# Optimization experiments

Measured on AMD Instinct MI355X. Metric: run time of the kernel, lower is better.

The kernel has to match this reference:

```python
import jax, jax.numpy as jnp
import numpy as np

VOCAB = 100000
EMB = 256
HID = 512
H = HID // 2            # per-direction hidden size
T_LEN = 2048
N_TAGS = 7
START, END = 5, 6
NEG = -10000.0


def setup_inputs() -> dict:
    key = jax.random.key(0)
    ks = jax.random.split(key, 16)
    n = lambda k, sh: jax.random.normal(k, sh, dtype=jnp.float32)
    bound = 1.0 / np.sqrt(H)  # torch LSTM/Linear-style init scale
    u = lambda k, sh: jax.random.uniform(k, sh, dtype=jnp.float32, minval=-bound, maxval=bound)
    transitions = n(ks[12], (N_TAGS, N_TAGS))
    transitions = transitions.at[:, START].set(NEG).at[END, :].set(NEG)
    return {
        "words": jax.random.randint(ks[0], (T_LEN,), 0, VOCAB),
        "embed": n(ks[1], (VOCAB + 1, EMB)),
        "W_ih_f": u(ks[2], (4 * H, EMB)),
        "W_hh_f": u(ks[3], (4 * H, H)),
        "b_ih_f": u(ks[4], (4 * H,)),
        "b_hh_f": u(ks[5], (4 * H,)),
        "W_ih_b": u(ks[6], (4 * H, EMB)),
        "W_hh_b": u(ks[7], (4 * H, H)),
        "b_ih_b": u(ks[8], (4 * H,)),
        "b_hh_b": u(ks[9], (4 * H,)),
        "W_out": u(ks[10], (N_TAGS, HID)),
        "b_out": u(ks[11], (N_TAGS,)),
        "transitions": transitions,
        "h0": n(ks[13], (2, H)),
        "c0": n(ks[14], (2, H)),
    }


def _lstm_dir(xs, h0, c0, Wih, Whh, bih, bhh):
    # xs: [T, EMB]; torch gate order i, f, g, o
    def step(carry, x):
        h, c = carry
        g = x @ Wih.T + bih + h @ Whh.T + bhh  # [4H]
        i, f, gg, o = jnp.split(g, 4)
        i, f, o = jax.nn.sigmoid(i), jax.nn.sigmoid(f), jax.nn.sigmoid(o)
        c = f * c + i * jnp.tanh(gg)
        h = o * jnp.tanh(c)
        return (h, c), h
    _, hs = jax.lax.scan(step, (h0, c0), xs)
    return hs  # [T, H]


def _features(words, embed, W_ih_f, W_hh_f, b_ih_f, b_hh_f,
              W_ih_b, W_hh_b, b_ih_b, b_hh_b, W_out, b_out, h0, c0):
    xs = embed[words]                                   # [T, EMB]
    hs_f = _lstm_dir(xs, h0[0], c0[0], W_ih_f, W_hh_f, b_ih_f, b_hh_f)
    hs_b = _lstm_dir(xs[::-1], h0[1], c0[1], W_ih_b, W_hh_b, b_ih_b, b_hh_b)[::-1]
    lstm_out = jnp.concatenate([hs_f, hs_b], axis=1)    # [T, HID]
    return lstm_out @ W_out.T + b_out                   # [T, N_TAGS]


def _viterbi(feats, transitions):
    init = jnp.full((N_TAGS,), NEG, dtype=feats.dtype).at[START].set(0.0)

    def vit_step(fv, feat):
        # torch code: next_tag_var[j] = forward_var + transitions[j]
        M = fv[None, :] + transitions          # [j, i] = fv[i] + T[j, i]
        bp = jnp.argmax(M, axis=1)             # [N_TAGS] best prev tag
        fv_new = jnp.max(M, axis=1) + feat
        return fv_new, bp

    fv, bptrs = jax.lax.scan(vit_step, init, feats)     # bptrs: [T, N_TAGS]
    terminal = fv + transitions[END]
    final_tag = jnp.argmax(terminal)
    path_score = terminal[final_tag]

    def back_step(tag, bp):
        return bp[tag], tag
    _start, path = jax.lax.scan(back_step, final_tag, bptrs, reverse=True)
    return path_score, path  # path: [T] tag ids (B/I/E/S/N = 0..4)


def reference(words, embed, W_ih_f, W_hh_f, b_ih_f, b_hh_f,
              W_ih_b, W_hh_b, b_ih_b, b_hh_b, W_out, b_out,
              transitions, h0, c0):
    feats = _features(words, embed, W_ih_f, W_hh_f, b_ih_f, b_hh_f,
                      W_ih_b, W_hh_b, b_ih_b, b_hh_b, W_out, b_out, h0, c0)
    return _viterbi(feats, transitions)
```

## Files before the change

kernel.cpp:

```cpp
#include <hip/hip_runtime.h>

typedef unsigned int u32;
typedef int v4i __attribute__((ext_vector_type(4)));

#define T_LEN 2048
#define NEG (-10000.0f)
#define WSCALE 2032.0f
#define HSCALE 127.0f
#define SCALE_INV (1.0f / (2032.0f * 127.0f))

__device__ __forceinline__ u32 rdlane_u32(u32 v, int lane) {
#if __has_builtin(__builtin_amdgcn_readlane)
  return (u32)__builtin_amdgcn_readlane((int)v, lane);
#else
  return (u32)__shfl((int)v, lane);
#endif
}

__device__ __forceinline__ float rdlane_f32(float v, int lane) {
  return __builtin_bit_cast(float, rdlane_u32(__builtin_bit_cast(u32, v), lane));
}

__device__ __forceinline__ void block_sync_lds() {
  asm volatile("s_waitcnt lgkmcnt(0)" ::: "memory");
  __builtin_amdgcn_s_barrier();
}

__device__ __forceinline__ v4i mfma_i8(v4i a, v4i b, v4i c) {
#if __has_builtin(__builtin_amdgcn_mfma_i32_16x16x64_i8)
  return __builtin_amdgcn_mfma_i32_16x16x64_i8(a, b, c, 0, 0, 0);
#else
  v4i d;
  asm("v_mfma_i32_16x16x64_i8 %0, %1, %2, %3"
      : "=&v"(d) : "v"(a), "v"(b), "v"(c));
  return d;
#endif
}

__global__ void pack_whh_i8(const float* __restrict__ Wf,
                            const float* __restrict__ Wb,
                            u32* __restrict__ WP) {
  int idx = blockIdx.x * 256 + threadIdx.x;
  int e  = idx & 3;
  int l  = (idx >> 2) & 63;
  int kt = (idx >> 8) & 3;
  int rt = (idx >> 10) & 63;
  int d  = (idx >> 16) & 1;
  int row = rt * 16 + (l & 15);
  int k0  = kt * 64 + (l >> 4) * 16 + e * 4;
  const float* W = d ? Wb : Wf;
  u32 p = 0;
  #pragma unroll
  for (int b = 0; b < 4; ++b) {
    float x = W[row * 256 + k0 + b];
    int q = (int)rintf(fminf(fmaxf(x * WSCALE, -127.f), 127.f));
    p |= (u32)(q & 255) << (8 * b);
  }
  WP[idx] = p;
}

__global__ void gather_kernel(const int* __restrict__ words,
                              const float* __restrict__ embed,
                              float* __restrict__ xs) {
  int t = blockIdx.x;
  int k = threadIdx.x;
  xs[t * 256 + k] = embed[(size_t)words[t] * 256 + k];
}

__global__ __launch_bounds__(256) void gemm_xw(
    const float* __restrict__ xs,
    const float* __restrict__ Wf, const float* __restrict__ Wb,
    const float* __restrict__ bihf, const float* __restrict__ bhhf,
    const float* __restrict__ bihb, const float* __restrict__ bhhb,
    float* __restrict__ XW) {
  __shared__ float lx[32 * 256];
  __shared__ float lw[32 * 132];
  const int tid = threadIdx.x;
  const int t0 = blockIdx.x * 32;
  const int g0 = blockIdx.y * 128;
  const int d  = blockIdx.z;
  const float* W = d ? Wb : Wf;

  #pragma unroll 4
  for (int r = 0; r < 32; ++r) lx[r * 256 + tid] = xs[(t0 + r) * 256 + tid];

  const int tg = tid & 31, tt = tid >> 5;
  float acc[4][4] = {};

  for (int kc = 0; kc < 8; ++kc) {
    __syncthreads();
    #pragma unroll
    for (int r2 = 0; r2 < 16; ++r2) {
      int gg = r2 * 8 + (tid >> 5);
      int k  = tid & 31;
      lw[k * 132 + gg] = W[(g0 + gg) * 256 + kc * 32 + k];
    }
    __syncthreads();
    #pragma unroll
    for (int k = 0; k < 32; ++k) {
      float4 wv = *(const float4*)&lw[k * 132 + tg * 4];
      #pragma unroll
      for (int a = 0; a < 4; ++a) {
        float xa = lx[(tt * 4 + a) * 256 + kc * 32 + k];
        acc[a][0] = fmaf(xa, wv.x, acc[a][0]);
        acc[a][1] = fmaf(xa, wv.y, acc[a][1]);
        acc[a][2] = fmaf(xa, wv.z, acc[a][2]);
        acc[a][3] = fmaf(xa, wv.w, acc[a][3]);
      }
    }
  }
  const float* bih = d ? bihb : bihf;
  const float* bhh = d ? bhhb : bhhf;
  int gcol = g0 + tg * 4;
  float bb[4];
  #pragma unroll
  for (int j = 0; j < 4; ++j) bb[j] = bih[gcol + j] + bhh[gcol + j];
  #pragma unroll
  for (int a = 0; a < 4; ++a) {
    size_t trow = (size_t)d * T_LEN + t0 + tt * 4 + a;
    #pragma unroll
    for (int j = 0; j < 4; ++j) {
      int g = gcol + j;
      XW[trow * 1024 + (g & 255) * 4 + (g >> 8)] = acc[a][j] + bb[j];
    }
  }
}

__global__ void __launch_bounds__(512)
__attribute__((amdgpu_waves_per_eu(2, 2)))
lstm_seq(
    const float* __restrict__ XW, float* __restrict__ HS,
    const u32* __restrict__ wpack,
    const float* __restrict__ h0, const float* __restrict__ c0) {
  __shared__ u32 smem[1152];
  const int t = threadIdx.x;
  const int d = blockIdx.x;
  const int lane = t & 63;
  const int w = t >> 6;
  const int c = t & 255;

  v4i A[8][4];
  {
    const v4i* AP = (const v4i*)wpack;
    #pragma unroll
    for (int j = 0; j < 8; ++j) {
      #pragma unroll
      for (int kt = 0; kt < 4; ++kt)
        A[j][kt] = AP[((d * 64 + w * 8 + j) * 4 + kt) * 64 + lane];
    }
  }

  unsigned char* H8b = (unsigned char*)smem;
  float cst = 0.f, h = 0.f;
  if (t < 256) {
    cst = c0[d * 256 + c];
    h   = h0[d * 256 + c];
    int hi = (int)rintf(fminf(fmaxf(h, -1.f), 1.f) * HSCALE);
    H8b[c] = (unsigned char)(hi & 255);
  }
  block_sync_lds();

  const char* sb = (const char*)smem;
  const int gq = (lane >> 4) * 16;
  char* gtp = (char*)smem + 512 + w * 512 + gq;

  const int delta = d ? -1024 : 1024;
  const float* xwp = XW + ((size_t)d * T_LEN + (d ? (T_LEN - 1) : 0)) * 1024 + c * 4;
  float4 xc = make_float4(0.f, 0.f, 0.f, 0.f);
  if (t < 256) xc = *(const float4*)xwp;

  for (int s = 0; s < T_LEN; ++s) {
    float4 xn = make_float4(0.f, 0.f, 0.f, 0.f);
    if (t < 256 && s < T_LEN - 1) { xwp += delta; xn = *(const float4*)xwp; }

    const char* hp = sb + (s & 1) * 256 + gq;
    v4i B0 = *(const v4i*)(hp);
    v4i B1 = *(const v4i*)(hp + 64);
    v4i B2 = *(const v4i*)(hp + 128);
    v4i B3 = *(const v4i*)(hp + 192);

    v4i D[8];
    #pragma unroll
    for (int j = 0; j < 8; ++j) {
      v4i acc = {0, 0, 0, 0};
      acc = mfma_i8(A[j][0], B0, acc);
      acc = mfma_i8(A[j][1], B1, acc);
      acc = mfma_i8(A[j][2], B2, acc);
      acc = mfma_i8(A[j][3], B3, acc);
      D[j] = acc;
    }
    if ((lane & 15) == 0) {
      #pragma unroll
      for (int j = 0; j < 8; ++j)
        *(v4i*)(gtp + j * 64) = D[j];
    }
    block_sync_lds();

    if (t < 256) {
      int aI = *(const int*)(sb + 512  + c * 4);
      int aF = *(const int*)(sb + 1536 + c * 4);
      int aG = *(const int*)(sb + 2560 + c * 4);
      int aO = *(const int*)(sb + 3584 + c * 4);
      float gi = fmaf((float)aI, SCALE_INV, xc.x);
      float gf = fmaf((float)aF, SCALE_INV, xc.y);
      float gc = fmaf((float)aG, SCALE_INV, xc.z);
      float go = fmaf((float)aO, SCALE_INV, xc.w);
      gi = 1.f / (1.f + __expf(-gi));
      gf = 1.f / (1.f + __expf(-gf));
      go = 1.f / (1.f + __expf(-go));
      gc = 1.f - 2.f / (__expf(2.f * gc) + 1.f);
      cst = gf * cst + gi * gc;
      float th = 1.f - 2.f / (__expf(2.f * cst) + 1.f);
      h = go * th;
      int hi = (int)rintf(h * HSCALE);
      H8b[((s + 1) & 1) * 256 + c] = (unsigned char)(hi & 255);
      const int tt = d ? (T_LEN - 1 - s) : s;
      HS[((size_t)d * T_LEN + tt) * 256 + c] = h;
    }
    block_sync_lds();
    xc = xn;
  }
}

__global__ void feats_kernel(const float* __restrict__ hs,
                             const float* __restrict__ wout,
                             const float* __restrict__ bout,
                             float* __restrict__ feats) {
  __shared__ float lf[16 * 257];
  __shared__ float lb[16 * 257];
  const int tid = threadIdx.x;
  const int t0 = blockIdx.x * 16;
  for (int i = tid; i < 16 * 256; i += 128) {
    int r = i >> 8, k = i & 255;
    lf[r * 257 + k] = hs[(size_t)(t0 + r) * 256 + k];
    lb[r * 257 + k] = hs[(size_t)T_LEN * 256 + (size_t)(t0 + r) * 256 + k];
  }
  __syncthreads();
  const int tl = tid >> 3, n = tid & 7;
  if (n < 7) {
    float acc = bout[n];
    #pragma unroll 8
    for (int k = 0; k < 256; ++k) acc = fmaf(lf[tl * 257 + k], wout[n * 512 + k], acc);
    #pragma unroll 8
    for (int k = 0; k < 256; ++k) acc = fmaf(lb[tl * 257 + k], wout[n * 512 + 256 + k], acc);
    feats[(t0 + tl) * 7 + n] = acc;
  }
}

__global__ __launch_bounds__(256) void viterbi_kernel(
    const float* __restrict__ feats,
    const float* __restrict__ trans,
    float* __restrict__ out) {
  extern __shared__ char vsm[];
  float*         fe = (float*)vsm;
  unsigned char* bp = (unsigned char*)(vsm + 57344);
  unsigned char* G  = (unsigned char*)(vsm + 73728);
  unsigned char* bt = (unsigned char*)(vsm + 73984);
  const int tid = threadIdx.x;

  for (int i = tid; i < T_LEN * 7; i += 256) fe[i] = feats[i];
  __syncthreads();

  if (tid < 64) {
    const int j  = tid;
    const int jc = (j < 7) ? j : 0;
    float Trow[7];
    #pragma unroll
    for (int i = 0; i < 7; ++i) Trow[i] = trans[jc * 7 + i];
    float fv = (j == 5) ? 0.0f : NEG;
    for (int t = 0; t < T_LEN; ++t) {
      float f0 = rdlane_f32(fv, 0), f1 = rdlane_f32(fv, 1), f2 = rdlane_f32(fv, 2),
            f3 = rdlane_f32(fv, 3), f4 = rdlane_f32(fv, 4), f5 = rdlane_f32(fv, 5),
            f6 = rdlane_f32(fv, 6);
      float v0 = f0 + Trow[0], v1 = f1 + Trow[1], v2 = f2 + Trow[2],
            v3 = f3 + Trow[3], v4 = f4 + Trow[4], v5 = f5 + Trow[5],
            v6 = f6 + Trow[6];
      bool c01 = v0 >= v1;  float m01 = c01 ? v0 : v1;  int i01 = c01 ? 0 : 1;
      bool c23 = v2 >= v3;  float m23 = c23 ? v2 : v3;  int i23 = c23 ? 2 : 3;
      bool c45 = v4 >= v5;  float m45 = c45 ? v4 : v5;  int i45 = c45 ? 4 : 5;
      bool cA  = m01 >= m23; float mA = cA ? m01 : m23; int iA = cA ? i01 : i23;
      bool cB  = m45 >= v6;  float mB = cB ? m45 : v6;  int iB = cB ? i45 : 6;
      bool cF  = mA >= mB;   float best = cF ? mA : mB; int bi = cF ? iA : iB;
      if (j < 7) bp[t * 8 + j] = (unsigned char)bi;
      fv = best + fe[t * 7 + jc];
    }
    float term = fv + trans[42 + jc];
    float best = rdlane_f32(term, 0); int btag = 0;
    #pragma unroll
    for (int i = 1; i < 7; ++i) {
      float ti = rdlane_f32(term, i);
      if (ti > best) { best = ti; btag = i; }
    }
    if (j == 0) {
      out[0] = best;
      bt[31] = (unsigned char)btag;
    }
  }
  __syncthreads();

  {
    const int s = tid >> 3, j = tid & 7;
    if (s < 32 && j < 7) {
      int g = j;
      for (int t = s * 64 + 63; t >= s * 64; --t) g = bp[t * 8 + g];
      G[s * 8 + j] = (unsigned char)g;
    }
  }
  __syncthreads();

  if (tid == 0) {
    int x = bt[31];
    for (int s = 31; s >= 1; --s) { x = G[s * 8 + x]; bt[s - 1] = (unsigned char)x; }
  }
  __syncthreads();

  if (tid < 32) {
    const int s = tid;
    int tag = bt[s];
    for (int t = s * 64 + 63; t >= s * 64; --t) {
      out[1 + t] = (float)tag;
      tag = bp[t * 8 + tag];
    }
  }
}

extern "C" void kernel_launch(void* const* d_in, const int* in_sizes, int n_in,
                              void* d_out, int out_size, void* d_ws, size_t ws_size,
                              hipStream_t stream) {
  const int*   words = (const int*)d_in[0];
  const float* embed = (const float*)d_in[1];
  const float* Wih_f = (const float*)d_in[2];
  const float* Whh_f = (const float*)d_in[3];
  const float* bih_f = (const float*)d_in[4];
  const float* bhh_f = (const float*)d_in[5];
  const float* Wih_b = (const float*)d_in[6];
  const float* Whh_b = (const float*)d_in[7];
  const float* bih_b = (const float*)d_in[8];
  const float* bhh_b = (const float*)d_in[9];
  const float* Wout  = (const float*)d_in[10];
  const float* bout  = (const float*)d_in[11];
  const float* trans = (const float*)d_in[12];
  const float* h0    = (const float*)d_in[13];
  const float* c0    = (const float*)d_in[14];

  float* ws = (float*)d_ws;
  float* XW = ws;
  float* HS = ws + 4194304;
  float* XS = ws + 5242880;
  float* FE = ws + 5767168;
  u32*   WP = (u32*)(ws + 5781504);

  pack_whh_i8<<<512, 256, 0, stream>>>(Whh_f, Whh_b, WP);
  gather_kernel<<<T_LEN, 256, 0, stream>>>(words, embed, XS);
  dim3 ggrid(T_LEN / 32, 1024 / 128, 2);
  gemm_xw<<<ggrid, 256, 0, stream>>>(XS, Wih_f, Wih_b, bih_f, bhh_f, bih_b, bhh_b, XW);
  lstm_seq<<<2, 512, 0, stream>>>(XW, HS, WP, h0, c0);
  feats_kernel<<<128, 128, 0, stream>>>(HS, Wout, bout, FE);
  viterbi_kernel<<<1, 256, 74048, stream>>>(FE, trans, (float*)d_out);
}
```

Before: 2.518 ms.

## Interleave gate rows so each wave computes its own cells, dropping a barrier

The packed recurrent weights are reordered so that each 16-row MFMA tile holds the i/f/g/o gate rows for four hidden units. Each wave then produces all four gates for its own 32 cells and reads them back from its private LDS region. This swaps one of the two per-step block barriers for a wave-local lgkmcnt wait, cutting block-wide synchronisation on the serial 2048-step recurrence. The gate-combine work is now spread as 32 active lanes in each of 8 waves rather than 4 fully active waves, which adds lane divergence per wave.

```diff
diff --git a/kernel.cpp b/kernel.cpp
--- a/kernel.cpp
+++ b/kernel.cpp
@@ -24,6 +24,10 @@
 __device__ __forceinline__ void block_sync_lds() {
   asm volatile("s_waitcnt lgkmcnt(0)" ::: "memory");
   __builtin_amdgcn_s_barrier();
+}
+
+__device__ __forceinline__ void wave_lds_fence() {
+  asm volatile("s_waitcnt lgkmcnt(0)" ::: "memory");
 }
 
 __device__ __forceinline__ v4i mfma_i8(v4i a, v4i b, v4i c) {
@@ -46,7 +50,8 @@
   int kt = (idx >> 8) & 3;
   int rt = (idx >> 10) & 63;
   int d  = (idx >> 16) & 1;
-  int row = rt * 16 + (l & 15);
+  int i   = l & 15;
+  int row = (i & 3) * 256 + rt * 4 + (i >> 2);
   int k0  = kt * 64 + (l >> 4) * 16 + e * 4;
   const float* W = d ? Wb : Wf;
   u32 p = 0;
@@ -137,7 +142,6 @@
   const int d = blockIdx.x;
   const int lane = t & 63;
   const int w = t >> 6;
-  const int c = t & 255;
 
   v4i A[8][4];
   {
@@ -151,8 +155,12 @@
   }
 
   unsigned char* H8b = (unsigned char*)smem;
+  char* GTw = (char*)smem + 512 + w * 512;
+  const bool cons = (lane < 32);
+  const int c = w * 32 + (lane & 31);
+
   float cst = 0.f, h = 0.f;
-  if (t < 256) {
+  if (cons) {
     cst = c0[d * 256 + c];
     h   = h0[d * 256 + c];
     int hi = (int)rintf(fminf(fmaxf(h, -1.f), 1.f) * HSCALE);
@@ -162,16 +170,18 @@
 
   const char* sb = (const char*)smem;
   const int gq = (lane >> 4) * 16;
-  char* gtp = (char*)smem + 512 + w * 512 + gq;
+  char* gtp = GTw + gq;
+  const char* grd = GTw + (lane & 31) * 16;
+  const v4i vzero = {0, 0, 0, 0};
 
   const int delta = d ? -1024 : 1024;
   const float* xwp = XW + ((size_t)d * T_LEN + (d ? (T_LEN - 1) : 0)) * 1024 + c * 4;
   float4 xc = make_float4(0.f, 0.f, 0.f, 0.f);
-  if (t < 256) xc = *(const float4*)xwp;
+  if (cons) xc = *(const float4*)xwp;
 
   for (int s = 0; s < T_LEN; ++s) {
     float4 xn = make_float4(0.f, 0.f, 0.f, 0.f);
-    if (t < 256 && s < T_LEN - 1) { xwp += delta; xn = *(const float4*)xwp; }
+    if (cons && s < T_LEN - 1) { xwp += delta; xn = *(const float4*)xwp; }
 
     const char* hp = sb + (s & 1) * 256 + gq;
     v4i B0 = *(const v4i*)(hp);
@@ -182,8 +192,7 @@
     v4i D[8];
     #pragma unroll
     for (int j = 0; j < 8; ++j) {
-      v4i acc = {0, 0, 0, 0};
-      acc = mfma_i8(A[j][0], B0, acc);
+      v4i acc = mfma_i8(A[j][0], B0, vzero);
       acc = mfma_i8(A[j][1], B1, acc);
       acc = mfma_i8(A[j][2], B2, acc);
       acc = mfma_i8(A[j][3], B3, acc);
@@ -194,17 +203,14 @@
       for (int j = 0; j < 8; ++j)
         *(v4i*)(gtp + j * 64) = D[j];
     }
-    block_sync_lds();
-
-    if (t < 256) {
-      int aI = *(const int*)(sb + 512  + c * 4);
-      int aF = *(const int*)(sb + 1536 + c * 4);
-      int aG = *(const int*)(sb + 2560 + c * 4);
-      int aO = *(const int*)(sb + 3584 + c * 4);
-      float gi = fmaf((float)aI, SCALE_INV, xc.x);
-      float gf = fmaf((float)aF, SCALE_INV, xc.y);
-      float gc = fmaf((float)aG, SCALE_INV, xc.z);
-      float go = fmaf((float)aO, SCALE_INV, xc.w);
+    wave_lds_fence();
+
+    if (cons) {
+      v4i gv = *(const v4i*)grd;
+      float gi = fmaf((float)gv.x, SCALE_INV, xc.x);
+      float gf = fmaf((float)gv.y, SCALE_INV, xc.y);
+      float gc = fmaf((float)gv.z, SCALE_INV, xc.z);
+      float go = fmaf((float)gv.w, SCALE_INV, xc.w);
       gi = 1.f / (1.f + __expf(-gi));
       gf = 1.f / (1.f + __expf(-gf));
       go = 1.f / (1.f + __expf(-go));
@@ -212,10 +218,10 @@
       cst = gf * cst + gi * gc;
       float th = 1.f - 2.f / (__expf(2.f * cst) + 1.f);
       h = go * th;
+      const int tt = d ? (T_LEN - 1 - s) : s;
+      HS[((size_t)d * T_LEN + tt) * 256 + c] = h;
       int hi = (int)rintf(h * HSCALE);
       H8b[((s + 1) & 1) * 256 + c] = (unsigned char)(hi & 255);
-      const int tt = d ? (T_LEN - 1 - s) : s;
-      HS[((size_t)d * T_LEN + tt) * 256 + c] = h;
     }
     block_sync_lds();
     xc = xn;
```

Result: faster. 2.466 ms (-2.1%).
